# Kernel optimization log

Measured on AMD Instinct MI355X. Metric: run time of the kernel, lower is better.

Reference implementation:

```python
import jax, jax.numpy as jnp
import numpy as np

N = 67108864  # 64M elements, ~256 MB fp32


def setup_inputs() -> dict:
    key = jax.random.key(0)
    x = jax.random.normal(key, (N,), dtype=jnp.float32)
    return {"x": x, "bins": 256, "min": -4, "max": 4}


def reference(x, bins, min, max):
    # Faithful jnp translation of torch.histc:
    #   bin width = (max - min) / bins
    #   values in [min, max] are counted; x == max falls in the last bin;
    #   values outside the range are dropped. Output dtype matches input (float).
    lo = jnp.float32(min)
    hi = jnp.float32(max)
    width = (hi - lo) / bins
    idx = jnp.floor((x - lo) / width).astype(jnp.int32)
    # right edge is inclusive -> goes to last bin
    idx = jnp.clip(idx, 0, bins - 1)
    in_range = (x >= lo) & (x <= hi)
    w = jnp.where(in_range, jnp.float32(1.0), jnp.float32(0.0))
    hist = jnp.zeros((bins,), dtype=jnp.float32).at[idx].add(w)
    return hist
```

## Files before the change

kernel.cpp:

```cpp
#include <hip/hip_runtime.h>

#define NBINS 256
#define TPB 256
#define NCOPY 4
#define CSTRIDE 264

typedef float f32x4 __attribute__((ext_vector_type(4)));

__global__ void zero_out_kernel(float* __restrict__ out) {
    out[threadIdx.x] = 0.0f;
}

__global__ __launch_bounds__(TPB) void hist_kernel(const float* __restrict__ x,
                                                   float* __restrict__ out,
                                                   int n) {
    __shared__ int lh[NCOPY * CSTRIDE];
    const int tid = threadIdx.x;
    int* __restrict__ myh = &lh[(tid >> 6) * CSTRIDE];

    for (int i = tid; i < NCOPY * CSTRIDE; i += TPB)
        lh[i] = 0;
    __syncthreads();

    const int gid    = blockIdx.x * TPB + tid;
    const int stride = gridDim.x * TPB;
    const int n4     = n >> 2;
    const f32x4* __restrict__ x4 = (const f32x4*)x;

#define PROC(f) {                                        \
        float _t = ((f) + 4.0f) * 32.0f;                 \
        int   _b = (int)_t;                              \
        _b = _b > 255 ? 255 : _b;                        \
        bool _ok = ((f) >= -4.0f) & ((f) <= 4.0f);       \
        _b = _ok ? _b : 256;                             \
        atomicAdd(&myh[_b], 1);                          \
    }

    int i = gid;
    for (; i + 3 * stride < n4; i += 4 * stride) {
        f32x4 a = __builtin_nontemporal_load(&x4[i]);
        f32x4 b = __builtin_nontemporal_load(&x4[i + stride]);
        f32x4 c = __builtin_nontemporal_load(&x4[i + 2 * stride]);
        f32x4 d = __builtin_nontemporal_load(&x4[i + 3 * stride]);
        PROC(a.x) PROC(a.y) PROC(a.z) PROC(a.w)
        PROC(b.x) PROC(b.y) PROC(b.z) PROC(b.w)
        PROC(c.x) PROC(c.y) PROC(c.z) PROC(c.w)
        PROC(d.x) PROC(d.y) PROC(d.z) PROC(d.w)
    }
    for (; i < n4; i += stride) {
        f32x4 a = __builtin_nontemporal_load(&x4[i]);
        PROC(a.x) PROC(a.y) PROC(a.z) PROC(a.w)
    }
    for (int j = (n4 << 2) + gid; j < n; j += stride) {
        float f = x[j];
        PROC(f)
    }
#undef PROC

    __syncthreads();

    int s = lh[0 * CSTRIDE + tid] + lh[1 * CSTRIDE + tid] +
            lh[2 * CSTRIDE + tid] + lh[3 * CSTRIDE + tid];
    if (s)
        atomicAdd(&out[tid], (float)s);
}

extern "C" void kernel_launch(void* const* d_in, const int* in_sizes, int n_in,
                              void* d_out, int out_size, void* d_ws, size_t ws_size,
                              hipStream_t stream) {
    const float* x = (const float*)d_in[0];
    float* out = (float*)d_out;
    const int n = in_sizes[0];

    zero_out_kernel<<<1, NBINS, 0, stream>>>(out);

    int n4 = n >> 2;
    long long want = ((long long)n4 + (long long)TPB * 4 - 1) / ((long long)TPB * 4);
    int blocks = (int)(want < 1 ? 1 : (want > 2048 ? 2048 : want));
    hist_kernel<<<blocks, TPB, 0, stream>>>(x, out, n);
}
```

Measured before the change: 79.29 us.

## Software-pipeline eight vector loads per thread and simplify bin arithmetic

The main loop now loads eight float4 vectors per iteration and prefetches the next eight into registers while the current batch is binned, so memory latency overlaps the LDS atomics. Nontemporal loads are replaced by plain loads. The bin calculation uses a single FMA, an unsigned conversion and an fabs range test. This raises register pressure, which may lower occupancy. The grid sizing now assumes eight vectors per thread, but with 64M elements it stays capped at 2048 blocks.

```diff
diff --git a/kernel.cpp b/kernel.cpp
--- a/kernel.cpp
+++ b/kernel.cpp
@@ -28,33 +28,56 @@
     const f32x4* __restrict__ x4 = (const f32x4*)x;
 
 #define PROC(f) {                                        \
-        float _t = ((f) + 4.0f) * 32.0f;                 \
-        int   _b = (int)_t;                              \
-        _b = _b > 255 ? 255 : _b;                        \
-        bool _ok = ((f) >= -4.0f) & ((f) <= 4.0f);       \
-        _b = _ok ? _b : 256;                             \
+        float _t = __builtin_fmaf((f), 32.0f, 128.0f);   \
+        unsigned _u = (unsigned)_t;                      \
+        _u = _u > 255u ? 255u : _u;                      \
+        bool _ok = __builtin_fabsf(f) <= 4.0f;           \
+        int _b = _ok ? (int)_u : 256;                    \
         atomicAdd(&myh[_b], 1);                          \
     }
+#define PROC4(a) { PROC(a.x) PROC(a.y) PROC(a.z) PROC(a.w) }
 
-    int i = gid;
-    for (; i + 3 * stride < n4; i += 4 * stride) {
-        f32x4 a = __builtin_nontemporal_load(&x4[i]);
-        f32x4 b = __builtin_nontemporal_load(&x4[i + stride]);
-        f32x4 c = __builtin_nontemporal_load(&x4[i + 2 * stride]);
-        f32x4 d = __builtin_nontemporal_load(&x4[i + 3 * stride]);
-        PROC(a.x) PROC(a.y) PROC(a.z) PROC(a.w)
-        PROC(b.x) PROC(b.y) PROC(b.z) PROC(b.w)
-        PROC(c.x) PROC(c.y) PROC(c.z) PROC(c.w)
-        PROC(d.x) PROC(d.y) PROC(d.z) PROC(d.w)
+    const int iters = n4 / (8 * stride);
+
+    if (iters > 0) {
+        int i = gid;
+        f32x4 a = x4[i];
+        f32x4 b = x4[i + stride];
+        f32x4 c = x4[i + 2 * stride];
+        f32x4 d = x4[i + 3 * stride];
+        f32x4 e = x4[i + 4 * stride];
+        f32x4 f = x4[i + 5 * stride];
+        f32x4 g = x4[i + 6 * stride];
+        f32x4 h = x4[i + 7 * stride];
+        for (int t = 1; t < iters; ++t) {
+            const int ni = i + 8 * stride;
+            f32x4 na = x4[ni];
+            f32x4 nb = x4[ni + stride];
+            f32x4 nc = x4[ni + 2 * stride];
+            f32x4 nd = x4[ni + 3 * stride];
+            f32x4 ne = x4[ni + 4 * stride];
+            f32x4 nf = x4[ni + 5 * stride];
+            f32x4 ng = x4[ni + 6 * stride];
+            f32x4 nh = x4[ni + 7 * stride];
+            PROC4(a) PROC4(b) PROC4(c) PROC4(d)
+            PROC4(e) PROC4(f) PROC4(g) PROC4(h)
+            a = na; b = nb; c = nc; d = nd;
+            e = ne; f = nf; g = ng; h = nh;
+            i = ni;
+        }
+        PROC4(a) PROC4(b) PROC4(c) PROC4(d)
+        PROC4(e) PROC4(f) PROC4(g) PROC4(h)
     }
-    for (; i < n4; i += stride) {
-        f32x4 a = __builtin_nontemporal_load(&x4[i]);
-        PROC(a.x) PROC(a.y) PROC(a.z) PROC(a.w)
+
+    for (int i2 = iters * 8 * stride + gid; i2 < n4; i2 += stride) {
+        f32x4 a = x4[i2];
+        PROC4(a)
     }
     for (int j = (n4 << 2) + gid; j < n; j += stride) {
-        float f = x[j];
-        PROC(f)
+        float f2 = x[j];
+        PROC(f2)
     }
+#undef PROC4
 #undef PROC
 
     __syncthreads();
@@ -75,7 +98,7 @@
     zero_out_kernel<<<1, NBINS, 0, stream>>>(out);
 
     int n4 = n >> 2;
-    long long want = ((long long)n4 + (long long)TPB * 4 - 1) / ((long long)TPB * 4);
+    long long want = ((long long)n4 + (long long)TPB * 8 - 1) / ((long long)TPB * 8);
     int blocks = (int)(want < 1 ? 1 : (want > 2048 ? 2048 : want));
     hist_kernel<<<blocks, TPB, 0, stream>>>(x, out, n);
 }
```

Result: faster. 76.31 us (-3.8%).
